# Kernel optimization log

Hardware: AMD Instinct MI355X
Metric: run time of the kernel (lower is better)

The kernel has to match this reference:

```python
import jax, jax.numpy as jnp
import numpy as np


def setup_inputs() -> dict:
    key = jax.random.key(0)
    ks = jax.random.split(key, 5)
    b, t, q_dim, kv_dim, h = 16, 128, 256, 64, 4
    c = t - 1
    q_x = jax.random.normal(ks[0], (b, t, q_dim), dtype=jnp.float32)
    kv_x = jax.random.normal(ks[1], (b, t, c, kv_dim), dtype=jnp.float32)
    # Linear weights stored as [in, out]; no biases (bias=False in torch module).
    sq = 1.0 / np.sqrt(q_dim)
    sk = 1.0 / np.sqrt(kv_dim)
    Wq = jax.random.uniform(ks[2], (q_dim, kv_dim * h), jnp.float32, -sq, sq)
    Wk = jax.random.uniform(ks[3], (kv_dim, kv_dim * h), jnp.float32, -sk, sk)
    Wv = jax.random.uniform(ks[4], (kv_dim, kv_dim * h), jnp.float32, -sk, sk)
    return {"q_x": q_x, "kv_x": kv_x, "Wq": Wq, "Wk": Wk, "Wv": Wv}


def reference(q_x, kv_x, Wq, Wk, Wv):
    b, t, c, k = kv_x.shape  # c = t - 1
    h = Wq.shape[1] // k
    # projections
    q = (q_x @ Wq).reshape(b, t, h, k)          # [b,t,h,k]
    keys = (kv_x @ Wk).reshape(b, t, c, h, k)   # [b,t,c,h,k]
    vals = (kv_x @ Wv).reshape(b, t, c, h, k)
    # per-token attention over the c-sized context
    scores = jnp.einsum('bthk,btchk->bthc', q, keys) / jnp.sqrt(jnp.float32(k))
    w = jax.nn.softmax(scores, axis=-1)          # softmax over context dim
    out = jnp.einsum('bthc,btchk->bthk', w, vals)
    return out.reshape(b, t, h * k)
```

## Files before the change

### kernel.cpp

```cpp
#include <hip/hip_runtime.h>
#include <math.h>

#define Bdim 16
#define Tdim 128
#define Cdim 127
#define Hdim 4
#define QD   256
#define HK   256
#define BT   (Bdim * Tdim)

#define DPP_XOR1 0xB1
#define DPP_XOR2 0x4E
template<int CTRL>
__device__ __forceinline__ float dpp_movf(float x) {
    return __int_as_float(__builtin_amdgcn_update_dpp(
        0, __float_as_int(x), CTRL, 0xF, 0xF, true));
}
__device__ __forceinline__ float dot4(float4 a, float4 b, float s) {
    return fmaf(a.x, b.x, fmaf(a.y, b.y, fmaf(a.z, b.z, fmaf(a.w, b.w, s))));
}
__device__ __forceinline__ float4 fma4(float e, float4 x, float4 v) {
    v.x = fmaf(e, x.x, v.x); v.y = fmaf(e, x.y, v.y);
    v.z = fmaf(e, x.z, v.z); v.w = fmaf(e, x.w, v.w);
    return v;
}
__device__ __forceinline__ float4 add4(float4 a, float4 b) {
    return make_float4(a.x + b.x, a.y + b.y, a.z + b.z, a.w + b.w);
}
__device__ __forceinline__ float4 shfl4(float4 v, int m) {
    return make_float4(__shfl_xor(v.x, m, 64), __shfl_xor(v.y, m, 64),
                       __shfl_xor(v.z, m, 64), __shfl_xor(v.w, m, 64));
}
__device__ __forceinline__ float4 sel4(int c, float4 a, float4 b) {
    return c ? a : b;
}

__global__ __launch_bounds__(256) void qk_fused(
        const float* __restrict__ q_x,
        const float* __restrict__ Wq,
        const float* __restrict__ Wk,
        float* __restrict__ qk) {
    __shared__ __align__(16) float q_s[4][256];
    __shared__ __align__(16) float p_s[4][4][68];
    int RB = blockIdx.x;
    int tid = threadIdx.x;
    {
        int r = tid >> 6, kq = tid & 63;
        *(float4*)&q_s[r][kq*4] =
            *(const float4*)(q_x + (size_t)(RB*4 + r) * QD + kq * 4);
    }
    __syncthreads();

    float acc[4] = {0.f, 0.f, 0.f, 0.f};
    #pragma unroll 4
    for (int i4 = 0; i4 < 64; ++i4) {
        float w0 = Wq[(size_t)(4*i4+0) * HK + tid];
        float w1 = Wq[(size_t)(4*i4+1) * HK + tid];
        float w2 = Wq[(size_t)(4*i4+2) * HK + tid];
        float w3 = Wq[(size_t)(4*i4+3) * HK + tid];
        #pragma unroll
        for (int r = 0; r < 4; ++r) {
            float4 qv = *(const float4*)&q_s[r][i4*4];
            acc[r] = fmaf(qv.x, w0, fmaf(qv.y, w1, fmaf(qv.z, w2, fmaf(qv.w, w3, acc[r]))));
        }
    }
    int h = tid >> 6, m = tid & 63;
    #pragma unroll
    for (int r = 0; r < 4; ++r) p_s[r][h][m] = acc[r];
    __syncthreads();

    const float4* wk4 = (const float4*)(Wk + (size_t)m * HK + h * 64);
    float4 wkr[16];
    #pragma unroll
    for (int j = 0; j < 16; ++j) wkr[j] = wk4[j];
    float a2[4] = {0.f, 0.f, 0.f, 0.f};
    #pragma unroll
    for (int j4 = 0; j4 < 16; ++j4) {
        #pragma unroll
        for (int r = 0; r < 4; ++r) {
            float4 pv = *(const float4*)&p_s[r][h][j4*4];
            a2[r] = fmaf(pv.x, wkr[j4].x, fmaf(pv.y, wkr[j4].y,
                    fmaf(pv.z, wkr[j4].z, fmaf(pv.w, wkr[j4].w, a2[r]))));
        }
    }
    #pragma unroll
    for (int r = 0; r < 4; ++r)
        qk[(size_t)(RB*4 + r) * HK + tid] = a2[r];
}

__global__ __launch_bounds__(256, 2) void attn_core(
        const float* __restrict__ kv_x,
        const float* __restrict__ qk_g,
        float* __restrict__ wx_buf,
        float* __restrict__ denom_buf) {
    int tid = threadIdx.x;
    int wv = tid >> 6, lane = tid & 63;
    int bt = blockIdx.x * 4 + wv;
    int r  = lane >> 2;
    int jq = lane & 3;
    const float* Xr = kv_x + (size_t)bt * (Cdim * 64);

    const float4* qb = (const float4*)(qk_g + (size_t)bt * HK);
    float4 Q00 = qb[ 0 + jq*4 + 0], Q01 = qb[ 0 + jq*4 + 1],
           Q02 = qb[ 0 + jq*4 + 2], Q03 = qb[ 0 + jq*4 + 3];
    float4 Q10 = qb[16 + jq*4 + 0], Q11 = qb[16 + jq*4 + 1],
           Q12 = qb[16 + jq*4 + 2], Q13 = qb[16 + jq*4 + 3];
    float4 Q20 = qb[32 + jq*4 + 0], Q21 = qb[32 + jq*4 + 1],
           Q22 = qb[32 + jq*4 + 2], Q23 = qb[32 + jq*4 + 3];
    float4 Q30 = qb[48 + jq*4 + 0], Q31 = qb[48 + jq*4 + 1],
           Q32 = qb[48 + jq*4 + 2], Q33 = qb[48 + jq*4 + 3];

    float4 V00={0,0,0,0},V01={0,0,0,0},V02={0,0,0,0},V03={0,0,0,0};
    float4 V10={0,0,0,0},V11={0,0,0,0},V12={0,0,0,0},V13={0,0,0,0};
    float4 V20={0,0,0,0},V21={0,0,0,0},V22={0,0,0,0},V23={0,0,0,0};
    float4 V30={0,0,0,0},V31={0,0,0,0},V32={0,0,0,0},V33={0,0,0,0};
    float d0=0.f, d1=0.f, d2=0.f, d3=0.f;
    float4 A0, A1, A2, A3, B0, B1, B2, B3;

#define LOADR(P0,P1,P2,P3,KK) do {                                           \
    int c_ = 16*(KK) + r;                                                    \
    const float4* xp_ = (const float4*)(Xr + (size_t)((c_ < Cdim) ? c_ : 0)  \
                                        * 64) + jq * 4;                      \
    P0 = xp_[0]; P1 = xp_[1]; P2 = xp_[2]; P3 = xp_[3];                      \
} while (0)

#define COMP(P0,P1,P2,P3,KK) do {                                            \
    float s0 = dot4(Q00,P0,0.f); s0 = dot4(Q01,P1,s0);                       \
    s0 = dot4(Q02,P2,s0); s0 = dot4(Q03,P3,s0);                              \
    float s1 = dot4(Q10,P0,0.f); s1 = dot4(Q11,P1,s1);                       \
    s1 = dot4(Q12,P2,s1); s1 = dot4(Q13,P3,s1);                              \
    float s2 = dot4(Q20,P0,0.f); s2 = dot4(Q21,P1,s2);                       \
    s2 = dot4(Q22,P2,s2); s2 = dot4(Q23,P3,s2);                              \
    float s3 = dot4(Q30,P0,0.f); s3 = dot4(Q31,P1,s3);                       \
    s3 = dot4(Q32,P2,s3); s3 = dot4(Q33,P3,s3);                              \
    s0 += dpp_movf<DPP_XOR1>(s0); s0 += dpp_movf<DPP_XOR2>(s0);              \
    s1 += dpp_movf<DPP_XOR1>(s1); s1 += dpp_movf<DPP_XOR2>(s1);              \
    s2 += dpp_movf<DPP_XOR1>(s2); s2 += dpp_movf<DPP_XOR2>(s2);              \
    s3 += dpp_movf<DPP_XOR1>(s3); s3 += dpp_movf<DPP_XOR2>(s3);              \
    bool vld_ = (16*(KK) + r) < Cdim;                                        \
    float e0 = vld_ ? __expf(s0 * 0.125f) : 0.f;                             \
    float e1 = vld_ ? __expf(s1 * 0.125f) : 0.f;                             \
    float e2 = vld_ ? __expf(s2 * 0.125f) : 0.f;                             \
    float e3 = vld_ ? __expf(s3 * 0.125f) : 0.f;                             \
    d0 += e0; d1 += e1; d2 += e2; d3 += e3;                                  \
    V00=fma4(e0,P0,V00); V01=fma4(e0,P1,V01);                                \
    V02=fma4(e0,P2,V02); V03=fma4(e0,P3,V03);                                \
    V10=fma4(e1,P0,V10); V11=fma4(e1,P1,V11);                                \
    V12=fma4(e1,P2,V12); V13=fma4(e1,P3,V13);                                \
    V20=fma4(e2,P0,V20); V21=fma4(e2,P1,V21);                                \
    V22=fma4(e2,P2,V22); V23=fma4(e2,P3,V23);                                \
    V30=fma4(e3,P0,V30); V31=fma4(e3,P1,V31);                                \
    V32=fma4(e3,P2,V32); V33=fma4(e3,P3,V33);                                \
} while (0)

    LOADR(A0,A1,A2,A3,0);
    LOADR(B0,B1,B2,B3,1);
    COMP (A0,A1,A2,A3,0);
    LOADR(A0,A1,A2,A3,2);
    COMP (B0,B1,B2,B3,1);
    LOADR(B0,B1,B2,B3,3);
    COMP (A0,A1,A2,A3,2);
    LOADR(A0,A1,A2,A3,4);
    COMP (B0,B1,B2,B3,3);
    LOADR(B0,B1,B2,B3,5);
    COMP (A0,A1,A2,A3,4);
    LOADR(A0,A1,A2,A3,6);
    COMP (B0,B1,B2,B3,5);
    LOADR(B0,B1,B2,B3,7);
    COMP (A0,A1,A2,A3,6);
    COMP (B0,B1,B2,B3,7);
#undef LOADR
#undef COMP

    int r0 = (lane >> 2) & 1, r1 = (lane >> 3) & 1;
    int r2 = (lane >> 4) & 1, r3 = (lane >> 5) & 1;
    float4 K00 = add4(sel4(r0, V01, V00), shfl4(sel4(r0, V00, V01), 4));
    float4 K01 = add4(sel4(r0, V03, V02), shfl4(sel4(r0, V02, V03), 4));
    float4 K10 = add4(sel4(r0, V11, V10), shfl4(sel4(r0, V10, V11), 4));
    float4 K11 = add4(sel4(r0, V13, V12), shfl4(sel4(r0, V12, V13), 4));
    float4 K20 = add4(sel4(r0, V21, V20), shfl4(sel4(r0, V20, V21), 4));
    float4 K21 = add4(sel4(r0, V23, V22), shfl4(sel4(r0, V22, V23), 4));
    float4 K30 = add4(sel4(r0, V31, V30), shfl4(sel4(r0, V30, V31), 4));
    float4 K31 = add4(sel4(r0, V33, V32), shfl4(sel4(r0, V32, V33), 4));
    float4 L0 = add4(sel4(r1, K01, K00), shfl4(sel4(r1, K00, K01), 8));
    float4 L1 = add4(sel4(r1, K11, K10), shfl4(sel4(r1, K10, K11), 8));
    float4 L2 = add4(sel4(r1, K21, K20), shfl4(sel4(r1, K20, K21), 8));
    float4 L3 = add4(sel4(r1, K31, K30), shfl4(sel4(r1, K30, K31), 8));
    float4 M0 = add4(sel4(r2, L1, L0), shfl4(sel4(r2, L0, L1), 16));
    float4 M1 = add4(sel4(r2, L3, L2), shfl4(sel4(r2, L2, L3), 16));
    float4 F = add4(sel4(r3, M1, M0), shfl4(sel4(r3, M0, M1), 32));

    #pragma unroll
    for (int m = 4; m <= 32; m <<= 1) {
        d0 += __shfl_xor(d0, m, 64); d1 += __shfl_xor(d1, m, 64);
        d2 += __shfl_xor(d2, m, 64); d3 += __shfl_xor(d3, m, 64);
    }

    int H  = (r3 << 1) | r2;
    int qo = (r1 << 1) | r0;
    ((float4*)(wx_buf + (size_t)bt * HK))[H * 16 + jq * 4 + qo] = F;
    if (lane == 0)
        *(float4*)(denom_buf + (size_t)bt * 4) = make_float4(d0, d1, d2, d3);
}

__global__ __launch_bounds__(256) void vproj(
        const float* __restrict__ wx_buf,
        const float* __restrict__ denom_buf,
        const float* __restrict__ Wv,
        float* __restrict__ out) {
    __shared__ __align__(16) float4 wx_s[4][64];
    __shared__ __align__(16) float4 dn_s[4];
    int B0 = blockIdx.x * 4;
    int tid = threadIdx.x;
    {
        int r = tid >> 6, l = tid & 63;
        wx_s[r][l] = ((const float4*)(wx_buf + (size_t)(B0 + r) * HK))[l];
    }
    if (tid < 4) dn_s[tid] = *(const float4*)(denom_buf + (size_t)(B0 + tid) * 4);
    __syncthreads();

    int h = tid >> 6;
    float wvr[64];
    #pragma unroll
    for (int j = 0; j < 64; ++j) wvr[j] = Wv[(size_t)j * HK + tid];
    #pragma unroll
    for (int r = 0; r < 4; ++r) {
        float acc = 0.f;
        #pragma unroll
        for (int j4 = 0; j4 < 16; ++j4) {
            float4 w4 = wx_s[r][h * 16 + j4];
            acc = fmaf(w4.x, wvr[j4*4+0], fmaf(w4.y, wvr[j4*4+1],
                  fmaf(w4.z, wvr[j4*4+2], fmaf(w4.w, wvr[j4*4+3], acc))));
        }
        float4 dn = dn_s[r];
        float d = (h == 0) ? dn.x : (h == 1) ? dn.y : (h == 2) ? dn.z : dn.w;
        out[(size_t)(B0 + r) * HK + tid] = acc / d;
    }
}

extern "C" void kernel_launch(void* const* d_in, const int* in_sizes, int n_in,
                              void* d_out, int out_size, void* d_ws, size_t ws_size,
                              hipStream_t stream) {
    const float* q_x  = (const float*)d_in[0];
    const float* kv_x = (const float*)d_in[1];
    const float* Wq   = (const float*)d_in[2];
    const float* Wk   = (const float*)d_in[3];
    const float* Wv   = (const float*)d_in[4];
    float* out = (float*)d_out;

    float* qk    = (float*)d_ws;
    float* wxb   = qk + (size_t)BT * HK;
    float* denom = wxb + (size_t)BT * HK;

    qk_fused <<<BT / 4, 256, 0, stream>>>(q_x, Wq, Wk, qk);
    attn_core<<<BT / 4, 256, 0, stream>>>(kv_x, qk, wxb, denom);
    vproj    <<<BT / 4, 256, 0, stream>>>(wxb, denom, Wv, out);
}
```

Baseline: 36.50 us.

## Fuse value projection into attention kernel and triple-buffer context loads

```diff
diff --git a/kernel.cpp b/kernel.cpp
--- a/kernel.cpp
+++ b/kernel.cpp
@@ -88,11 +88,12 @@
         qk[(size_t)(RB*4 + r) * HK + tid] = a2[r];
 }
 
-__global__ __launch_bounds__(256, 2) void attn_core(
+__global__ __launch_bounds__(256, 2) void attn_fused(
         const float* __restrict__ kv_x,
         const float* __restrict__ qk_g,
-        float* __restrict__ wx_buf,
-        float* __restrict__ denom_buf) {
+        const float* __restrict__ Wv,
+        float* __restrict__ out) {
+    __shared__ __align__(16) float4 wx_s[4][64];
     int tid = threadIdx.x;
     int wv = tid >> 6, lane = tid & 63;
     int bt = blockIdx.x * 4 + wv;
@@ -115,7 +116,7 @@
     float4 V20={0,0,0,0},V21={0,0,0,0},V22={0,0,0,0},V23={0,0,0,0};
     float4 V30={0,0,0,0},V31={0,0,0,0},V32={0,0,0,0},V33={0,0,0,0};
     float d0=0.f, d1=0.f, d2=0.f, d3=0.f;
-    float4 A0, A1, A2, A3, B0, B1, B2, B3;
+    float4 A0, A1, A2, A3, B0, B1, B2, B3, C0, C1, C2, C3;
 
 #define LOADR(P0,P1,P2,P3,KK) do {                                           \
     int c_ = 16*(KK) + r;                                                    \
@@ -155,18 +156,18 @@
 
     LOADR(A0,A1,A2,A3,0);
     LOADR(B0,B1,B2,B3,1);
+    LOADR(C0,C1,C2,C3,2);
     COMP (A0,A1,A2,A3,0);
-    LOADR(A0,A1,A2,A3,2);
+    LOADR(A0,A1,A2,A3,3);
     COMP (B0,B1,B2,B3,1);
-    LOADR(B0,B1,B2,B3,3);
-    COMP (A0,A1,A2,A3,2);
-    LOADR(A0,A1,A2,A3,4);
-    COMP (B0,B1,B2,B3,3);
-    LOADR(B0,B1,B2,B3,5);
-    COMP (A0,A1,A2,A3,4);
+    LOADR(B0,B1,B2,B3,4);
+    COMP (C0,C1,C2,C3,2);
+    LOADR(C0,C1,C2,C3,5);
+    COMP (A0,A1,A2,A3,3);
     LOADR(A0,A1,A2,A3,6);
-    COMP (B0,B1,B2,B3,5);
+    COMP (B0,B1,B2,B3,4);
     LOADR(B0,B1,B2,B3,7);
+    COMP (C0,C1,C2,C3,5);
     COMP (A0,A1,A2,A3,6);
     COMP (B0,B1,B2,B3,7);
 #undef LOADR
@@ -198,43 +199,27 @@
 
     int H  = (r3 << 1) | r2;
     int qo = (r1 << 1) | r0;
-    ((float4*)(wx_buf + (size_t)bt * HK))[H * 16 + jq * 4 + qo] = F;
-    if (lane == 0)
-        *(float4*)(denom_buf + (size_t)bt * 4) = make_float4(d0, d1, d2, d3);
-}
-
-__global__ __launch_bounds__(256) void vproj(
-        const float* __restrict__ wx_buf,
-        const float* __restrict__ denom_buf,
-        const float* __restrict__ Wv,
-        float* __restrict__ out) {
-    __shared__ __align__(16) float4 wx_s[4][64];
-    __shared__ __align__(16) float4 dn_s[4];
-    int B0 = blockIdx.x * 4;
-    int tid = threadIdx.x;
+    wx_s[wv][H * 16 + jq * 4 + qo] = F;
+
     {
-        int r = tid >> 6, l = tid & 63;
-        wx_s[r][l] = ((const float4*)(wx_buf + (size_t)(B0 + r) * HK))[l];
-    }
-    if (tid < 4) dn_s[tid] = *(const float4*)(denom_buf + (size_t)(B0 + tid) * 4);
-    __syncthreads();
-
-    int h = tid >> 6;
-    float wvr[64];
-    #pragma unroll
-    for (int j = 0; j < 64; ++j) wvr[j] = Wv[(size_t)j * HK + tid];
-    #pragma unroll
-    for (int r = 0; r < 4; ++r) {
-        float acc = 0.f;
+        float inv0 = 1.f / d0, inv1 = 1.f / d1, inv2 = 1.f / d2, inv3 = 1.f / d3;
+        float* obt = out + (size_t)bt * HK;
         #pragma unroll
-        for (int j4 = 0; j4 < 16; ++j4) {
-            float4 w4 = wx_s[r][h * 16 + j4];
-            acc = fmaf(w4.x, wvr[j4*4+0], fmaf(w4.y, wvr[j4*4+1],
-                  fmaf(w4.z, wvr[j4*4+2], fmaf(w4.w, wvr[j4*4+3], acc))));
+        for (int p = 0; p < 4; ++p) {
+            const float* wvc = Wv + p * 64 + lane;
+            float acc = 0.f;
+            #pragma unroll
+            for (int j4 = 0; j4 < 16; ++j4) {
+                float4 w4 = wx_s[wv][p * 16 + j4];
+                acc = fmaf(w4.x, wvc[(size_t)(j4*4+0) * HK],
+                      fmaf(w4.y, wvc[(size_t)(j4*4+1) * HK],
+                      fmaf(w4.z, wvc[(size_t)(j4*4+2) * HK],
+                      fmaf(w4.w, wvc[(size_t)(j4*4+3) * HK], acc))));
+            }
+            float inv = (p == 0) ? inv0 : (p == 1) ? inv1
+                      : (p == 2) ? inv2 : inv3;
+            obt[p * 64 + lane] = acc * inv;
         }
-        float4 dn = dn_s[r];
-        float d = (h == 0) ? dn.x : (h == 1) ? dn.y : (h == 2) ? dn.z : dn.w;
-        out[(size_t)(B0 + r) * HK + tid] = acc / d;
     }
 }
 
@@ -248,11 +233,8 @@
     const float* Wv   = (const float*)d_in[4];
     float* out = (float*)d_out;
 
-    float* qk    = (float*)d_ws;
-    float* wxb   = qk + (size_t)BT * HK;
-    float* denom = wxb + (size_t)BT * HK;
+    float* qk = (float*)d_ws;
 
     qk_fused <<<BT / 4, 256, 0, stream>>>(q_x, Wq, Wk, qk);
-    attn_core<<<BT / 4, 256, 0, stream>>>(kv_x, qk, wxb, denom);
-    vproj    <<<BT / 4, 256, 0, stream>>>(wxb, denom, Wv, out);
-}
+    attn_fused<<<BT / 4, 256, 0, stream>>>(kv_x, qk, Wv, out);
+}
```

Result: no change. 36.62 us (+0.3%).
